# Optimization experiments

Hardware: AMD Instinct MI355X
Metric: run time of the kernel (lower is better)

Reference implementation:

```python
import jax, jax.numpy as jnp
import numpy as np
from jax import lax

INPUT_SIZE = 512
THRESHOLD = 0.5
IOU_TH = 0.3
MAX_ROIS = 32   # py_cpu_nms(...)[:32]
ROI = 7
NEG = jnp.float32(-1e30)


def _make_anchors(fh, fw, stride):
    # 3 scales x 3 ratios = 9 anchors per cell, laid out in (h, w, anchor)
    # order to match permute(0,2,3,1).view(-1) of the conv heads.
    scales = np.array([32.0, 64.0, 128.0])
    ratios = np.array([0.5, 1.0, 2.0])
    ws = (scales[:, None] * np.sqrt(ratios)[None, :]).reshape(-1)
    hs = (scales[:, None] / np.sqrt(ratios)[None, :]).reshape(-1)
    cy = (np.arange(fh) + 0.5) * stride
    cx = (np.arange(fw) + 0.5) * stride
    CX, CY = np.meshgrid(cx, cy)
    CX = CX[..., None]; CY = CY[..., None]
    a = np.stack([CX - ws / 2, CY - hs / 2, CX + ws / 2, CY + hs / 2], axis=-1)
    return jnp.asarray(a.reshape(-1, 4), jnp.float32)


def setup_inputs() -> dict:
    key = jax.random.key(0)
    k1, k2, k3 = jax.random.split(key, 3)
    B, C, FH, FW, A, stride = 4, 256, 64, 64, 9, 8
    featureMap = jax.random.normal(k1, (B, C, FH, FW), jnp.float32)
    # small init so sigmoid scores spread across threshold and exp(tw) stays sane
    w_cls = jax.random.normal(k2, (A, C, 3, 3), jnp.float32) * 0.05
    w_loc = jax.random.normal(k3, (4 * A, C, 3, 3), jnp.float32) * 0.01
    prior_anchor = _make_anchors(FH, FW, stride)
    return {"featureMap": featureMap, "prior_anchor": prior_anchor,
            "w_cls": w_cls, "w_loc": w_loc, "stride": stride}


def _conv(x, w):
    return lax.conv_general_dilated(x, w, (1, 1), "SAME",
                                    dimension_numbers=("NCHW", "OIHW", "NCHW"))


def _decode(loc, anchors):
    aw = anchors[:, 2] - anchors[:, 0]
    ah = anchors[:, 3] - anchors[:, 1]
    acx = anchors[:, 0] + 0.5 * aw
    acy = anchors[:, 1] + 0.5 * ah
    cx = acx + loc[:, 0] * aw
    cy = acy + loc[:, 1] * ah
    w = aw * jnp.exp(loc[:, 2])
    h = ah * jnp.exp(loc[:, 3])
    return jnp.stack([cx - 0.5 * w, cy - 0.5 * h, cx + 0.5 * w, cy + 0.5 * h], axis=1)


def _iou_one(box, boxes):
    xx1 = jnp.maximum(box[0], boxes[:, 0]); yy1 = jnp.maximum(box[1], boxes[:, 1])
    xx2 = jnp.minimum(box[2], boxes[:, 2]); yy2 = jnp.minimum(box[3], boxes[:, 3])
    inter = jnp.clip(xx2 - xx1, 0) * jnp.clip(yy2 - yy1, 0)
    a1 = (box[2] - box[0]) * (box[3] - box[1])
    a2 = (boxes[:, 2] - boxes[:, 0]) * (boxes[:, 3] - boxes[:, 1])
    return inter / (a1 + a2 - inter + 1e-9)


def _nms(boxes, scores, valid):
    # greedy NMS, fixed MAX_ROIS rounds (== sort-by-score py_cpu_nms + [:32])
    N = scores.shape[0]
    s0 = jnp.where(valid, scores, -1.0)

    def body(i, carry):
        s, picks, ok = carry
        idx = jnp.argmax(s)
        good = s[idx] > 0.0
        picks = picks.at[i].set(idx.astype(jnp.int32))
        ok = ok.at[i].set(good)
        sup = (_iou_one(boxes[idx], boxes) > IOU_TH) | (jnp.arange(N) == idx)
        return (jnp.where(sup, -1.0, s), picks, ok)

    _, picks, ok = lax.fori_loop(
        0, MAX_ROIS, body,
        (s0, jnp.zeros(MAX_ROIS, jnp.int32), jnp.zeros(MAX_ROIS, bool)))
    return picks, ok


def _ceil_div(a, b):
    return -(-a // b)


def _adaptive_maxpool(feat, box):
    # feat: [C, FH, FW]; box: int32 [x1, y1, x2, y2] in feature-map coords.
    # Faithful F.adaptive_max_pool2d bins: start=floor(i*h/7), end=ceil((i+1)*h/7).
    FH, FW = feat.shape[1], feat.shape[2]
    x1, y1, x2, y2 = box[0], box[1], box[2], box[3]
    h = y2 - y1; w = x2 - x1
    i = jnp.arange(ROI)
    rs = y1 + (i * h) // ROI; re = y1 + _ceil_div((i + 1) * h, ROI)
    cs = x1 + (i * w) // ROI; ce = x1 + _ceil_div((i + 1) * w, ROI)
    hh = jnp.arange(FH); ww = jnp.arange(FW)
    rm = jnp.where((hh >= rs[:, None]) & (hh < re[:, None]), 0.0, NEG)  # [7, FH]
    cm = jnp.where((ww >= cs[:, None]) & (ww < ce[:, None]), 0.0, NEG)  # [7, FW]
    t = jnp.max(feat[None] + rm[:, None, :, None], axis=2)              # [7, C, FW]
    out = jnp.max(t[:, None] + cm[None, :, None, :], axis=3)            # [7, 7, C]
    return jnp.transpose(out, (2, 0, 1))                                # [C, 7, 7]


def reference(featureMap, prior_anchor, w_cls, w_loc, stride):
    B, C, FH, FW = featureMap.shape
    cls = jax.nn.sigmoid(_conv(featureMap, w_cls))                      # [B, A, FH, FW]
    cls = jnp.transpose(cls, (0, 2, 3, 1)).reshape(B, -1)               # [B, N]
    loc = jnp.transpose(_conv(featureMap, w_loc), (0, 2, 3, 1)).reshape(B, -1, 4)
    boxes = jax.vmap(_decode, in_axes=(0, None))(loc, prior_anchor)     # [B, N, 4]
    boxes = jnp.clip(boxes, 0.0, float(INPUT_SIZE))                     # clamp(0, input_size)
    valid = (cls > THRESHOLD) \
          & (boxes[..., 2] - boxes[..., 0] >= 2 * stride) \
          & (boxes[..., 3] - boxes[..., 1] >= 2 * stride)
    picks, ok = jax.vmap(_nms)(boxes, cls, valid)                       # [B, 32]
    sel_boxes = jnp.take_along_axis(boxes, picks[..., None], axis=1)    # [B, 32, 4]
    sel_scores = jnp.take_along_axis(cls, picks, axis=1)                # [B, 32]
    eval_boxes = jnp.where(
        ok[..., None],
        jnp.concatenate([sel_boxes, sel_scores[..., None]], axis=-1), 0.0)
    # src_coordinate.int() / stride -> integer feature-map coords
    ib = sel_boxes.astype(jnp.int32) // stride
    fx1 = jnp.clip(ib[..., 0], 0, FW - 1); fy1 = jnp.clip(ib[..., 1], 0, FH - 1)
    fx2 = jnp.clip(ib[..., 2], fx1 + 1, FW); fy2 = jnp.clip(ib[..., 3], fy1 + 1, FH)
    fb = jnp.stack([fx1, fy1, fx2, fy2], axis=-1).reshape(-1, 4)        # [B*32, 4]
    img = jnp.repeat(jnp.arange(B), MAX_ROIS)
    rois = lax.map(lambda a: _adaptive_maxpool(featureMap[a[1]], a[0]), (fb, img))
    rois = jnp.where(ok.reshape(-1)[:, None, None, None], rois, 0.0)    # [B*32, 256, 7, 7]
    return eval_boxes, ok, rois
```

## Files before the change

kernel.cpp:

```cpp
#include <hip/hip_runtime.h>
#include <hip/hip_bf16.h>

#define FHH 64
#define FWW 64
#define CIN 256
#define NB 4
#define NA 9
#define NANCH 36864
#define NPOS 4096
#define OC_TOTAL 45
#define OCP 48
#define MAXROIS 32
#define ROI 7
#define NEGV -1e30f
#define NCHUNK 576
#define NTH 16
#define CAP 1024

typedef unsigned long long u64;

__device__ __constant__ const float TH_LADDER[NTH] = {
    0.9999f, 0.9998f, 0.9995f, 0.999f, 0.998f, 0.997f, 0.995f, 0.993f,
    0.99f, 0.987f, 0.984f, 0.98f, 0.975f, 0.97f, 0.96f, 0.0f};

__device__ __forceinline__ void pick_threshold(
    const int* __restrict__ gcnt, int b, int cap,
    float* T, int* C, int* V, int* frc)
{
    int bestc = 0; float bt = TH_LADDER[0];
#pragma unroll
    for (int i = 0; i < NTH; ++i) {
        int c = gcnt[b * NTH + i];
        if (c <= cap && c > bestc) { bestc = c; bt = TH_LADDER[i]; }
    }
    int f = (gcnt[b * NTH + 0] > cap) ? 1 : 0;
    if (f) { bestc = cap; bt = TH_LADDER[0]; }
    *T = bt; *C = bestc; *V = gcnt[b * NTH + NTH - 1]; *frc = f;
}

__global__ __launch_bounds__(256) void wtrans_kernel(
    const float* __restrict__ wcls,
    const float* __restrict__ wloc,
    float* __restrict__ wT,
    int* __restrict__ gcnt)
{
    if (blockIdx.x == 0 && threadIdx.x < NB * NTH) gcnt[threadIdx.x] = 0;
    int idx = blockIdx.x * 256 + threadIdx.x;
    int o = idx % 48;
    int rest = idx / 48;
    int tap = rest % 9;
    int c = rest / 9;
    float v = 0.f;
    if (o < OC_TOTAL) {
        v = (o < NA) ? wcls[((size_t)o * CIN + c) * 9 + tap]
                     : wloc[((size_t)(o - NA) * CIN + c) * 9 + tap];
    }
    wT[idx] = v;
}

__global__ __launch_bounds__(256) void conv_kernel(
    const float* __restrict__ feat,
    const float* __restrict__ wT,
    float* __restrict__ partial,
    int nkg, int cpk)
{
    __shared__ float flds[16][18][20];

    int blk = blockIdx.x;
    int low = blk & 7;
    int rest = blk >> 3;
    int kg = rest % nkg;
    int uhi = rest / nkg;
    int unit = uhi * 8 + low;
    int b = unit >> 4;
    int tile = unit & 15;

    int ty0 = (tile >> 2) * 16;
    int tx0 = (tile & 3) * 16;

    int pb = threadIdx.x & 63;
    int q = __builtin_amdgcn_readfirstlane(threadIdx.x >> 6);
    int ry0 = (pb >> 3) * 2;
    int rx0 = (pb & 7) * 2;

    int cbase = kg * cpk;

    float acc[2][2][12];
#pragma unroll
    for (int py = 0; py < 2; ++py)
#pragma unroll
        for (int px = 0; px < 2; ++px)
#pragma unroll
            for (int o = 0; o < 12; ++o) acc[py][px][o] = 0.f;

    for (int c0 = 0; c0 < cpk; c0 += 16) {
        __syncthreads();
        for (int idx = threadIdx.x; idx < 16 * 324; idx += 256) {
            int c = idx / 324;
            int r = idx - c * 324;
            int y = r / 18;
            int x = r - y * 18;
            int gy = ty0 + y - 1;
            int gx = tx0 + x - 1;
            float v = 0.f;
            if ((unsigned)gy < FHH && (unsigned)gx < FWW)
                v = feat[((size_t)(b * CIN + cbase + c0 + c) * FHH + gy) * FWW + gx];
            flds[c][y][x] = v;
        }
        __syncthreads();

        const float* wq = wT + (size_t)(cbase + c0) * 432 + q * 12;
        for (int c = 0; c < 16; ++c) {
            float f[4][4];
#pragma unroll
            for (int r = 0; r < 4; ++r) {
                float2 a0 = *(const float2*)&flds[c][ry0 + r][rx0];
                float2 a1 = *(const float2*)&flds[c][ry0 + r][rx0 + 2];
                f[r][0] = a0.x; f[r][1] = a0.y; f[r][2] = a1.x; f[r][3] = a1.y;
            }
#pragma unroll
            for (int tap = 0; tap < 9; ++tap) {
                int dy = tap / 3, dx = tap % 3;
                const float* wp = wq + (c * 9 + tap) * 48;
                float w[12];
#pragma unroll
                for (int o = 0; o < 12; ++o) w[o] = wp[o];
#pragma unroll
                for (int py = 0; py < 2; ++py)
#pragma unroll
                for (int px = 0; px < 2; ++px) {
                    float fv = f[py + dy][px + dx];
#pragma unroll
                    for (int o = 0; o < 12; ++o)
                        acc[py][px][o] += fv * w[o];
                }
            }
        }
    }

    float* pout = partial + ((size_t)kg * NB + b) * OCP * NPOS;
#pragma unroll
    for (int o = 0; o < 12; ++o) {
        int oo = q * 12 + o;
        float* op = pout + (size_t)oo * NPOS;
#pragma unroll
        for (int py = 0; py < 2; ++py)
#pragma unroll
        for (int px = 0; px < 2; ++px) {
            int pos = (ty0 + ry0 + py) * FWW + (tx0 + rx0 + px);
            op[pos] = acc[py][px][o];
        }
    }
}

__global__ __launch_bounds__(256) void decode_kernel(
    const float* __restrict__ partial,
    const float* __restrict__ anchors,
    const int* __restrict__ stridep,
    float* __restrict__ boxes,
    float* __restrict__ scores,
    int* __restrict__ gcnt,
    int* __restrict__ gcount,
    int nkg)
{
    __shared__ int hcnt[NTH];
    if (threadIdx.x < NTH) hcnt[threadIdx.x] = 0;
    if (blockIdx.x == 0 && threadIdx.x < NB) gcount[threadIdx.x] = 0;
    __syncthreads();

    int t = blockIdx.x * 256 + threadIdx.x;
    int pos = t & (NPOS - 1);
    int ba = t >> 12;
    int b = ba / 9;
    int a = ba - b * 9;

    float cls = 0.f, l0 = 0.f, l1 = 0.f, l2 = 0.f, l3 = 0.f;
    for (int kg = 0; kg < nkg; ++kg) {
        const float* pk = partial + ((size_t)kg * NB + b) * OCP * NPOS;
        cls += pk[(size_t)a * NPOS + pos];
        l0 += pk[(size_t)(NA + a * 4 + 0) * NPOS + pos];
        l1 += pk[(size_t)(NA + a * 4 + 1) * NPOS + pos];
        l2 += pk[(size_t)(NA + a * 4 + 2) * NPOS + pos];
        l3 += pk[(size_t)(NA + a * 4 + 3) * NPOS + pos];
    }

    float sig = 1.f / (1.f + expf(-cls));
    int n = pos * NA + a;
    const float* an = anchors + (size_t)n * 4;
    float ax1 = an[0], ay1 = an[1], ax2 = an[2], ay2 = an[3];
    float aw = ax2 - ax1, ah = ay2 - ay1;
    float acx = ax1 + 0.5f * aw, acy = ay1 + 0.5f * ah;
    float cx = acx + l0 * aw;
    float cy = acy + l1 * ah;
    float w = aw * expf(l2);
    float h = ah * expf(l3);
    float x1 = fminf(fmaxf(cx - 0.5f * w, 0.f), 512.f);
    float y1 = fminf(fmaxf(cy - 0.5f * h, 0.f), 512.f);
    float x2 = fminf(fmaxf(cx + 0.5f * w, 0.f), 512.f);
    float y2 = fminf(fmaxf(cy + 0.5f * h, 0.f), 512.f);
    int stride = stridep[0];
    float msz = 2.f * (float)stride;
    bool valid = (sig > 0.5f) && ((x2 - x1) >= msz) && ((y2 - y1) >= msz);
    ((float4*)boxes)[(size_t)b * NANCH + n] = make_float4(x1, y1, x2, y2);
    scores[(size_t)b * NANCH + n] = valid ? sig : -1.0f;

#pragma unroll
    for (int i = 0; i < NTH; ++i) {
        u64 mb = __ballot(valid && sig >= TH_LADDER[i]);
        if ((threadIdx.x & 63) == 0 && mb)
            atomicAdd(&hcnt[i], (int)__popcll(mb));
    }
    __syncthreads();
    if (threadIdx.x < NTH && hcnt[threadIdx.x])
        atomicAdd(&gcnt[b * NTH + threadIdx.x], hcnt[threadIdx.x]);
}

__global__ __launch_bounds__(256) void nms_compact_kernel(
    const float* __restrict__ scores,
    const int* __restrict__ gcnt,
    int* __restrict__ gcount,
    u64* __restrict__ candkey,
    int cap)
{
    __shared__ int lcnt;
    __shared__ int wbase[4];
    __shared__ int gbase;
    int t = blockIdx.x * 256 + threadIdx.x;
    int b = t / NANCH;
    int j = t - b * NANCH;
    int lane = threadIdx.x & 63;
    int w = threadIdx.x >> 6;
    if (threadIdx.x == 0) lcnt = 0;
    __syncthreads();

    float T; int C, V, frc;
    pick_threshold(gcnt, b, cap, &T, &C, &V, &frc);

    float v = scores[t];
    bool p = (v > 0.f) && (v >= T);
    u64 m = __ballot(p);
    int cnt = (int)__popcll(m);
    if (lane == 0) wbase[w] = atomicAdd(&lcnt, cnt);
    __syncthreads();
    if (threadIdx.x == 0) gbase = lcnt ? atomicAdd(&gcount[b], lcnt) : 0;
    __syncthreads();
    if (p) {
        int off = (int)__popcll(m & ((1ULL << lane) - 1ULL));
        int slot = gbase + wbase[w] + off;
        if (slot < cap)
            candkey[(size_t)b * cap + slot] =
                ((u64)__float_as_uint(v) << 32) | (unsigned int)(~j);
    }
}

__device__ __forceinline__ void write_outputs(
    int b, int i, bool okv, int idx, float sc,
    const float4* Bb4, const int* stridep,
    float* d_out, int* ifb, int* iok)
{
    float4 bb = Bb4[idx];
    float* eb = d_out + ((size_t)b * MAXROIS + i) * 5;
    eb[0] = okv ? bb.x : 0.f;
    eb[1] = okv ? bb.y : 0.f;
    eb[2] = okv ? bb.z : 0.f;
    eb[3] = okv ? bb.w : 0.f;
    eb[4] = okv ? sc : 0.f;
    d_out[NB * MAXROIS * 5 + b * MAXROIS + i] = okv ? 1.f : 0.f;
    int st = stridep[0];
    int fx1 = min(max(((int)bb.x) / st, 0), FWW - 1);
    int fy1 = min(max(((int)bb.y) / st, 0), FHH - 1);
    int fx2 = min(max(((int)bb.z) / st, fx1 + 1), FWW);
    int fy2 = min(max(((int)bb.w) / st, fy1 + 1), FHH);
    int r = b * MAXROIS + i;
    ifb[r * 4 + 0] = fx1;
    ifb[r * 4 + 1] = fy1;
    ifb[r * 4 + 2] = fx2;
    ifb[r * 4 + 3] = fy2;
    iok[r] = okv ? 1 : 0;
}

__global__ __launch_bounds__(512) void nms_sortscan_kernel(
    const u64* __restrict__ candkey,
    const float* __restrict__ boxes,
    const int* __restrict__ gcnt,
    const int* __restrict__ stridep,
    float* __restrict__ d_out,
    int* __restrict__ ifb, int* __restrict__ iok, int* __restrict__ flag,
    int cap)
{
    __shared__ u64 skey[CAP];
    __shared__ float4 box_l[CAP];
    __shared__ u64 mask[CAP / 64];
    __shared__ int picks[MAXROIS];
    __shared__ int np_sh;

    int b = blockIdx.x;
    int tid = threadIdx.x;
    int lane = tid & 63;
    if (tid == 0) np_sh = 0;

    float T; int C, V, frc;
    pick_threshold(gcnt, b, cap, &T, &C, &V, &frc);

    int CSZ = 64;
    while (CSZ < C) CSZ <<= 1;

    for (int j = tid; j < CSZ; j += 512)
        skey[j] = (j < C) ? candkey[(size_t)b * cap + j] : 0ULL;

    int prev_cross = 1;
    for (int kk = 2; kk <= CSZ; kk <<= 1) {
        for (int jj = kk >> 1; jj > 0; jj >>= 1) {
            int cross = (jj >= 128) ? 1 : 0;
            if (cross || prev_cross) __syncthreads();
            for (int tt = tid; tt < (CSZ >> 1); tt += 512) {
                int i = ((tt & ~(jj - 1)) << 1) | (tt & (jj - 1));
                int l = i + jj;
                u64 a = skey[i], c2 = skey[l];
                bool up = ((i & kk) == 0);
                bool sw = up ? (a < c2) : (a > c2);
                if (sw) { skey[i] = c2; skey[l] = a; }
            }
            prev_cross = cross;
        }
    }
    __syncthreads();

    const float4* Bb4 = (const float4*)(boxes + (size_t)b * NANCH * 4);
    for (int j = tid; j < C; j += 512) {
        int id = (int)(~((unsigned int)(skey[j] & 0xFFFFFFFFULL)));
        box_l[j] = Bb4[id];
    }
    if (tid < CAP / 64) {
        int base = tid * 64;
        u64 m0;
        if (base >= C) m0 = ~0ULL;
        else if (base + 64 > C) m0 = ~((1ULL << (C - base)) - 1ULL);
        else m0 = 0ULL;
        mask[tid] = m0;
    }
    __syncthreads();

    for (int round = 0; round < MAXROIS; ++round) {
        u64 mw = (lane < CAP / 64) ? mask[lane] : ~0ULL;
        int bpos = __ffsll((u64)(~mw));
        int cand = bpos ? lane * 64 + bpos - 1 : 0x7FFFFFFF;
#pragma unroll
        for (int off = 32; off >= 1; off >>= 1)
            cand = min(cand, __shfl_xor(cand, off));
        int pj = cand;
        if (pj == 0x7FFFFFFF) break;
        if (tid == 0) {
            picks[round] = pj;
            np_sh = round + 1;
            atomicOr(&mask[pj >> 6], 1ULL << (pj & 63));
        }
        float4 pb = box_l[pj];
        float parea = (pb.z - pb.x) * (pb.w - pb.y);
        int j0 = tid * 2;
        u64 curm = mask[tid >> 5];
        u64 addm = 0ULL;
#pragma unroll
        for (int d = 0; d < 2; ++d) {
            int j = j0 + d;
            if (j > pj && j < C && !((curm >> (j & 63)) & 1ULL)) {
                float4 bb2 = box_l[j];
                float xx1 = fmaxf(pb.x, bb2.x), yy1 = fmaxf(pb.y, bb2.y);
                float xx2 = fminf(pb.z, bb2.z), yy2 = fminf(pb.w, bb2.w);
                float inter = fmaxf(xx2 - xx1, 0.f) * fmaxf(yy2 - yy1, 0.f);
                float a2 = (bb2.z - bb2.x) * (bb2.w - bb2.y);
                float iou = inter / (parea + a2 - inter + 1e-9f);
                if (iou > 0.3f) addm |= 1ULL << (j & 63);
            }
        }
        if (addm) atomicOr(&mask[tid >> 5], addm);
        __syncthreads();
    }
    __syncthreads();

    int np = np_sh;
    bool need_fb = frc || (np < MAXROIS && V > C);
    if (tid == 0) flag[b] = need_fb ? 1 : 0;
    if (!need_fb && tid < MAXROIS) {
        int i = tid;
        bool okv = i < np;
        int slot = okv ? picks[i] : 0;
        u64 k = skey[slot];
        int idx = okv ? (int)(~((unsigned int)(k & 0xFFFFFFFFULL))) : 0;
        float sc = okv ? __uint_as_float((unsigned int)(k >> 32)) : 0.f;
        write_outputs(b, i, okv, idx, sc, Bb4, stridep, d_out, ifb, iok);
    }
}

__global__ __launch_bounds__(1024) void nms_fallback_kernel(
    const float* __restrict__ boxes,
    const float* __restrict__ scores,
    const int* __restrict__ stridep,
    float* __restrict__ d_out,
    int* __restrict__ ifb,
    int* __restrict__ iok,
    const int* __restrict__ flag)
{
    __shared__ float s[NANCH];
    __shared__ float2 cmax[NCHUNK];
    __shared__ int   picks_sh[MAXROIS];
    __shared__ float pscore_sh[MAXROIS];

    int b = blockIdx.x;
    if (flag[b] == 0) return;

    const float4* Bb4 = (const float4*)(boxes + (size_t)b * NANCH * 4);
    const float* Sb = scores + (size_t)b * NANCH;
    int lane = threadIdx.x & 63;
    int w = threadIdx.x >> 6;

    for (int k = 0; k < 36; ++k) {
        int ch = w * 36 + k;
        int j = ch * 64 + lane;
        float v = Sb[j];
        s[j] = v;
        float bv = v; int bi = j;
#pragma unroll
        for (int off = 32; off >= 1; off >>= 1) {
            float ov = __shfl_xor(bv, off);
            int   oi = __shfl_xor(bi, off);
            if (ov > bv || (ov == bv && oi < bi)) { bv = ov; bi = oi; }
        }
        if (lane == 0) cmax[ch] = make_float2(bv, __int_as_float(bi));
    }
    __syncthreads();
    if (w != 0) return;

    float px1 = 0.f, py1 = 0.f, px2 = 0.f, py2 = 0.f, parea = 0.f;
    int np = 0;
    while (np < MAXROIS) {
        float bv = -2.f; int bi = 0x7fffffff;
#pragma unroll
        for (int k = 0; k < 9; ++k) {
            float2 cm = cmax[lane * 9 + k];
            int ci = __float_as_int(cm.y);
            if (cm.x > bv || (cm.x == bv && ci < bi)) { bv = cm.x; bi = ci; }
        }
#pragma unroll
        for (int off = 32; off >= 1; off >>= 1) {
            float ov = __shfl_xor(bv, off);
            int   oi = __shfl_xor(bi, off);
            if (ov > bv || (ov == bv && oi < bi)) { bv = ov; bi = oi; }
        }
        if (bv <= 0.f) break;
        int fi = bi; float fs = bv;

        float4 cbb = Bb4[fi];

        bool sup = false;
        if (lane < np) {
            float xx1 = fmaxf(px1, cbb.x), yy1 = fmaxf(py1, cbb.y);
            float xx2 = fminf(px2, cbb.z), yy2 = fminf(py2, cbb.w);
            float inter = fmaxf(xx2 - xx1, 0.f) * fmaxf(yy2 - yy1, 0.f);
            float a2 = (cbb.z - cbb.x) * (cbb.w - cbb.y);
            float iou = inter / (parea + a2 - inter + 1e-9f);
            sup = iou > 0.3f;
        }
        u64 m = __ballot(sup);

        int ch = fi >> 6;
        int j = ch * 64 + lane;
        float sv = (j == fi) ? -1.f : s[j];
        if (j == fi) s[j] = -1.f;
        float nv = sv; int ni = j;
#pragma unroll
        for (int off = 32; off >= 1; off >>= 1) {
            float ov = __shfl_xor(nv, off);
            int   oi = __shfl_xor(ni, off);
            if (ov > nv || (ov == nv && oi < ni)) { nv = ov; ni = oi; }
        }
        if (lane == 0) cmax[ch] = make_float2(nv, __int_as_float(ni));

        if (m == 0ULL) {
            if (lane == np) {
                px1 = cbb.x; py1 = cbb.y; px2 = cbb.z; py2 = cbb.w;
                parea = (px2 - px1) * (py2 - py1);
            }
            picks_sh[np] = fi;
            pscore_sh[np] = fs;
            ++np;
        }
    }

    if (lane < MAXROIS) {
        int i = lane;
        bool okv = i < np;
        int idx = okv ? picks_sh[i] : 0;
        float sc = okv ? pscore_sh[i] : 0.f;
        write_outputs(b, i, okv, idx, sc, Bb4, stridep, d_out, ifb, iok);
    }
}

__global__ __launch_bounds__(256) void roi_kernel(
    const float* __restrict__ feat,
    const int* __restrict__ ifb,
    const int* __restrict__ iok,
    float* __restrict__ out_rois)
{
    int t = blockIdx.x * 256 + threadIdx.x;
    int bin = t % 49;
    int rc = t / 49;
    int c = rc & 255;
    int r = rc >> 8;
    int i = bin / 7;
    int j = bin - i * 7;

    if (!iok[r]) { out_rois[t] = 0.f; return; }

    int x1 = ifb[r * 4 + 0];
    int y1 = ifb[r * 4 + 1];
    int x2 = ifb[r * 4 + 2];
    int y2 = ifb[r * 4 + 3];
    int h = y2 - y1;
    int w = x2 - x1;
    int b = r >> 5;

    int rs = y1 + (i * h) / ROI;
    int re = y1 + ((i + 1) * h + ROI - 1) / ROI;
    int cs = x1 + (j * w) / ROI;
    int ce = x1 + ((j + 1) * w + ROI - 1) / ROI;

    const float* F = feat + (size_t)(b * CIN + c) * NPOS;
    float m = NEGV;
    for (int y = rs; y < re; ++y) {
        const float* row = F + y * FWW;
        for (int x = cs; x < ce; ++x) m = fmaxf(m, row[x]);
    }
    out_rois[t] = m;
}

extern "C" void kernel_launch(void* const* d_in, const int* in_sizes, int n_in,
                              void* d_out, int out_size, void* d_ws, size_t ws_size,
                              hipStream_t stream) {
    const float* feat    = (const float*)d_in[0];
    const float* anchors = (const float*)d_in[1];
    const float* wcls    = (const float*)d_in[2];
    const float* wloc    = (const float*)d_in[3];
    const int*   stridep = (const int*)d_in[4];
    float* out = (float*)d_out;
    float* ws  = (float*)d_ws;

    const size_t P1 = (size_t)NB * OCP * NPOS;
    const size_t WTN = 256 * 9 * 48;
    const int cap = CAP;

    auto need = [&](int nk) -> size_t {
        size_t f = P1 * nk
                 + 589824 + 147456 + WTN
                 + (size_t)NB * cap * 2
                 + 2048;
        return f * 4;
    };
    int nkg = 16;
    if (ws_size < need(16)) {
        if (ws_size >= need(8)) { nkg = 8; }
        else { nkg = 4; }
    }

    float* partial   = ws;
    float* boxes     = partial + P1 * nkg;
    float* scores    = boxes + (size_t)NB * NANCH * 4;
    float* wT        = scores + (size_t)NB * NANCH;
    u64*   candkey   = (u64*)(wT + WTN);
    float* tailf     = (float*)(candkey + (size_t)NB * cap);
    int*   ifb       = (int*)tailf;
    int*   iok       = ifb + 512;
    int*   flag      = iok + 128;
    int*   gcnt      = flag + 4;
    int*   gcount    = gcnt + 64;

    wtrans_kernel<<<432, 256, 0, stream>>>(wcls, wloc, wT, gcnt);
    conv_kernel<<<64 * nkg, 256, 0, stream>>>(feat, wT, partial, nkg, CIN / nkg);
    decode_kernel<<<(NB * NANCH) / 256, 256, 0, stream>>>(partial, anchors, stridep, boxes, scores, gcnt, gcount, nkg);
    nms_compact_kernel<<<(NB * NANCH) / 256, 256, 0, stream>>>(scores, gcnt, gcount, candkey, cap);
    nms_sortscan_kernel<<<NB, 512, 0, stream>>>(candkey, boxes, gcnt, stridep, out, ifb, iok, flag, cap);
    nms_fallback_kernel<<<NB, 1024, 0, stream>>>(boxes, scores, stridep, out, ifb, iok, flag);
    roi_kernel<<<(NB * MAXROIS * CIN * 49) / 256, 256, 0, stream>>>(feat, ifb, iok, out + NB * MAXROIS * 5 + NB * MAXROIS);
}
```

Before: 137.2 us.

## Fuse candidate compaction into sort-scan kernel and halve conv K-split

Removes the separate compaction kernel and its global candidate buffer. Each per-image sort-scan block now scans all 36864 scores itself, using a wave ballot and a shared-memory atomic to compact candidates straight into shared memory. This drops one launch and a global round trip, but only 4 blocks now do the compaction scan serially. The conv K-split default also drops from 16 to 8 groups, which changes the conv grid size and the partial-sum reduction work in decode.

```diff
diff --git a/kernel.cpp b/kernel.cpp
--- a/kernel.cpp
+++ b/kernel.cpp
@@ -160,12 +160,10 @@
     float* __restrict__ boxes,
     float* __restrict__ scores,
     int* __restrict__ gcnt,
-    int* __restrict__ gcount,
     int nkg)
 {
     __shared__ int hcnt[NTH];
     if (threadIdx.x < NTH) hcnt[threadIdx.x] = 0;
-    if (blockIdx.x == 0 && threadIdx.x < NB) gcount[threadIdx.x] = 0;
     __syncthreads();
 
     int t = blockIdx.x * 256 + threadIdx.x;
@@ -215,44 +213,6 @@
         atomicAdd(&gcnt[b * NTH + threadIdx.x], hcnt[threadIdx.x]);
 }
 
-__global__ __launch_bounds__(256) void nms_compact_kernel(
-    const float* __restrict__ scores,
-    const int* __restrict__ gcnt,
-    int* __restrict__ gcount,
-    u64* __restrict__ candkey,
-    int cap)
-{
-    __shared__ int lcnt;
-    __shared__ int wbase[4];
-    __shared__ int gbase;
-    int t = blockIdx.x * 256 + threadIdx.x;
-    int b = t / NANCH;
-    int j = t - b * NANCH;
-    int lane = threadIdx.x & 63;
-    int w = threadIdx.x >> 6;
-    if (threadIdx.x == 0) lcnt = 0;
-    __syncthreads();
-
-    float T; int C, V, frc;
-    pick_threshold(gcnt, b, cap, &T, &C, &V, &frc);
-
-    float v = scores[t];
-    bool p = (v > 0.f) && (v >= T);
-    u64 m = __ballot(p);
-    int cnt = (int)__popcll(m);
-    if (lane == 0) wbase[w] = atomicAdd(&lcnt, cnt);
-    __syncthreads();
-    if (threadIdx.x == 0) gbase = lcnt ? atomicAdd(&gcount[b], lcnt) : 0;
-    __syncthreads();
-    if (p) {
-        int off = (int)__popcll(m & ((1ULL << lane) - 1ULL));
-        int slot = gbase + wbase[w] + off;
-        if (slot < cap)
-            candkey[(size_t)b * cap + slot] =
-                ((u64)__float_as_uint(v) << 32) | (unsigned int)(~j);
-    }
-}
-
 __device__ __forceinline__ void write_outputs(
     int b, int i, bool okv, int idx, float sc,
     const float4* Bb4, const int* stridep,
@@ -280,7 +240,7 @@
 }
 
 __global__ __launch_bounds__(512) void nms_sortscan_kernel(
-    const u64* __restrict__ candkey,
+    const float* __restrict__ scores,
     const float* __restrict__ boxes,
     const int* __restrict__ gcnt,
     const int* __restrict__ stridep,
@@ -293,20 +253,43 @@
     __shared__ u64 mask[CAP / 64];
     __shared__ int picks[MAXROIS];
     __shared__ int np_sh;
+    __shared__ int cpos;
 
     int b = blockIdx.x;
     int tid = threadIdx.x;
     int lane = tid & 63;
-    if (tid == 0) np_sh = 0;
+    if (tid == 0) { np_sh = 0; cpos = 0; }
+    __syncthreads();
 
     float T; int C, V, frc;
     pick_threshold(gcnt, b, cap, &T, &C, &V, &frc);
 
+    const float4* Sb4 = (const float4*)(scores + (size_t)b * NANCH);
+#pragma unroll
+    for (int k = 0; k < NANCH / 4 / 512; ++k) {
+        float4 v4 = Sb4[k * 512 + tid];
+#pragma unroll
+        for (int d = 0; d < 4; ++d) {
+            float v = (d == 0) ? v4.x : (d == 1) ? v4.y : (d == 2) ? v4.z : v4.w;
+            int j = (k * 512 + tid) * 4 + d;
+            bool p = (v > 0.f) && (v >= T);
+            u64 m = __ballot(p);
+            int base = 0;
+            if (lane == 0 && m) base = atomicAdd(&cpos, (int)__popcll(m));
+            base = __shfl(base, 0);
+            if (p) {
+                int off = (int)__popcll(m & ((1ULL << lane) - 1ULL));
+                int slot = base + off;
+                if (slot < cap)
+                    skey[slot] = ((u64)__float_as_uint(v) << 32) | (unsigned int)(~j);
+            }
+        }
+    }
+    __syncthreads();
+
     int CSZ = 64;
     while (CSZ < C) CSZ <<= 1;
-
-    for (int j = tid; j < CSZ; j += 512)
-        skey[j] = (j < C) ? candkey[(size_t)b * cap + j] : 0ULL;
+    for (int j = C + tid; j < CSZ; j += 512) skey[j] = 0ULL;
 
     int prev_cross = 1;
     for (int kk = 2; kk <= CSZ; kk <<= 1) {
@@ -552,33 +535,26 @@
     auto need = [&](int nk) -> size_t {
         size_t f = P1 * nk
                  + 589824 + 147456 + WTN
-                 + (size_t)NB * cap * 2
                  + 2048;
         return f * 4;
     };
-    int nkg = 16;
-    if (ws_size < need(16)) {
-        if (ws_size >= need(8)) { nkg = 8; }
-        else { nkg = 4; }
-    }
+    int nkg = 8;
+    if (ws_size < need(8)) nkg = 4;
 
     float* partial   = ws;
     float* boxes     = partial + P1 * nkg;
     float* scores    = boxes + (size_t)NB * NANCH * 4;
     float* wT        = scores + (size_t)NB * NANCH;
-    u64*   candkey   = (u64*)(wT + WTN);
-    float* tailf     = (float*)(candkey + (size_t)NB * cap);
+    float* tailf     = wT + WTN;
     int*   ifb       = (int*)tailf;
     int*   iok       = ifb + 512;
     int*   flag      = iok + 128;
     int*   gcnt      = flag + 4;
-    int*   gcount    = gcnt + 64;
 
     wtrans_kernel<<<432, 256, 0, stream>>>(wcls, wloc, wT, gcnt);
     conv_kernel<<<64 * nkg, 256, 0, stream>>>(feat, wT, partial, nkg, CIN / nkg);
-    decode_kernel<<<(NB * NANCH) / 256, 256, 0, stream>>>(partial, anchors, stridep, boxes, scores, gcnt, gcount, nkg);
-    nms_compact_kernel<<<(NB * NANCH) / 256, 256, 0, stream>>>(scores, gcnt, gcount, candkey, cap);
-    nms_sortscan_kernel<<<NB, 512, 0, stream>>>(candkey, boxes, gcnt, stridep, out, ifb, iok, flag, cap);
+    decode_kernel<<<(NB * NANCH) / 256, 256, 0, stream>>>(partial, anchors, stridep, boxes, scores, gcnt, nkg);
+    nms_sortscan_kernel<<<NB, 512, 0, stream>>>(scores, boxes, gcnt, stridep, out, ifb, iok, flag, cap);
     nms_fallback_kernel<<<NB, 1024, 0, stream>>>(boxes, scores, stridep, out, ifb, iok, flag);
     roi_kernel<<<(NB * MAXROIS * CIN * 49) / 256, 256, 0, stream>>>(feat, ifb, iok, out + NB * MAXROIS * 5 + NB * MAXROIS);
 }
```

New measurement: 154.0 us. +12.3%, slower.
